# Kernel optimization log

Hardware: AMD Instinct MI355X
Metric: run time of the kernel (lower is better)

Reference implementation:

```python
import jax, jax.numpy as jnp
import numpy as np

B, L, D, H = 4, 2048, 256, 8
FF = 128  # ff_intermediary_depth hard-coded in module
EPS = 1e-5


def layer_norm(x, g, b):
    mu = jnp.mean(x, axis=-1, keepdims=True)
    var = jnp.mean(jnp.square(x - mu), axis=-1, keepdims=True)
    return (x - mu) * jax.lax.rsqrt(var + EPS) * g + b


def setup_inputs() -> dict:
    key = jax.random.key(0)
    ks = jax.random.split(key, 8)
    s = 1.0 / np.sqrt(D)
    return {
        "seq": jax.random.normal(ks[0], (B, L, D), dtype=jnp.float32),
        "Wq": jax.random.normal(ks[1], (D, D * H), dtype=jnp.float32) * s,
        "Wk": jax.random.normal(ks[2], (D, D * H), dtype=jnp.float32) * s,
        "Wv": jax.random.normal(ks[3], (D, D * H), dtype=jnp.float32) * s,
        "Wo": jax.random.normal(ks[4], (D * H, D), dtype=jnp.float32) * (1.0 / np.sqrt(D * H)),
        "ln1_g": jnp.ones((D,), jnp.float32),
        "ln1_b": jnp.zeros((D,), jnp.float32),
        "W1": jax.random.normal(ks[5], (D, FF), dtype=jnp.float32) * s,
        "b1": jnp.zeros((FF,), jnp.float32),
        "W2": jax.random.normal(ks[6], (FF, D), dtype=jnp.float32) * (1.0 / np.sqrt(FF)),
        "b2": jnp.zeros((D,), jnp.float32),
        "ln2_g": jnp.ones((D,), jnp.float32),
        "ln2_b": jnp.zeros((D,), jnp.float32),
    }


def reference(seq, Wq, Wk, Wv, Wo, ln1_g, ln1_b, W1, b1, W2, b2, ln2_g, ln2_b):
    b, l, d = seq.shape
    # per-head dim equals full depth d (module quirk)
    q = (seq @ Wq).reshape(b, l, H, d)
    k = (seq @ Wk).reshape(b, l, H, d)
    v = (seq @ Wv).reshape(b, l, H, d)
    scores = jnp.einsum('bqhd,bkhd->bhqk', q, k) / jnp.sqrt(jnp.float32(d))
    a = jax.nn.softmax(scores, axis=-1)
    heads = jnp.einsum('bhqk,bkhd->bqhd', a, v).reshape(b, l, H * d)
    att_out = heads @ Wo
    x = layer_norm(seq + att_out, ln1_g, ln1_b)
    ff = jax.nn.relu(x @ W1 + b1) @ W2 + b2
    return layer_norm(x + ff, ln2_g, ln2_b)
```

## Files before the change

kernel.cpp:

```cpp
#include <hip/hip_runtime.h>


typedef unsigned short u16;
typedef unsigned int   u32;
typedef __bf16 bf16x8 __attribute__((ext_vector_type(8)));
typedef float  f32x4  __attribute__((ext_vector_type(4)));

#define MFMA(a, b, c) __builtin_amdgcn_mfma_f32_16x16x32_bf16(a, b, c, 0, 0, 0)

__device__ __forceinline__ float b2f(u16 h) {
  return __uint_as_float(((u32)h) << 16);
}
__device__ __forceinline__ u16 f2b(float f) {
  u32 u = __float_as_uint(f);
  u += 0x7FFFu + ((u >> 16) & 1u);
  return (u16)(u >> 16);
}
__device__ __forceinline__ bf16x8 ldb8(const u16* p) { return *(const bf16x8*)p; }

typedef const __attribute__((address_space(1))) u32* gas1_t;
typedef __attribute__((address_space(3))) u32* las3_t;
__device__ __forceinline__ void gload_lds16(const u16* g, u16* lds_base) {
  __builtin_amdgcn_global_load_lds((gas1_t)(const void*)g,
                                   (las3_t)(void*)lds_base, 16, 0, 0);
}

__device__ __forceinline__ int detect_f32(const void* seq) {
  const u32* s = (const u32*)seq;
  int cnt = 0;
  #pragma unroll
  for (int i = 0; i < 64; i++) {
    u32 e = (s[i] >> 7) & 0xFFu;
    cnt += (e >= 100u && e <= 140u) ? 1 : 0;
  }
  return cnt < 48;
}

__device__ __forceinline__ u16 ldw(const void* W, size_t idx, int isf32) {
  return isf32 ? f2b(((const float*)W)[idx]) : ((const u16*)W)[idx];
}

__global__ __launch_bounds__(256) void ingest_kernel(
    const void* __restrict__ seq, const void* __restrict__ g1,
    const void* __restrict__ be1, const void* __restrict__ b1,
    const void* __restrict__ b2v, const void* __restrict__ g2,
    const void* __restrict__ be2, u16* __restrict__ sbuf,
    u16* __restrict__ vecs) {
  int isf32 = detect_f32(seq);
  int bx = blockIdx.x, tid = threadIdx.x;
  if (bx < 2048) {
    size_t i = (size_t)bx * 1024 + tid * 4;
    if (isf32) {
      const float* sp = (const float*)seq;
      u16 o0 = f2b(sp[i]), o1 = f2b(sp[i + 1]), o2 = f2b(sp[i + 2]), o3 = f2b(sp[i + 3]);
      uint2 ov; ov.x = (u32)o0 | ((u32)o1 << 16); ov.y = (u32)o2 | ((u32)o3 << 16);
      *(uint2*)(sbuf + i) = ov;
    } else {
      *(uint2*)(sbuf + i) = ((const uint2*)seq)[i >> 2];
    }
  } else {
    int t = bx - 2048;
    const void* src; int n;
    switch (t) {
      case 0: src = g1;  n = 256; break;
      case 1: src = be1; n = 256; break;
      case 2: src = b1;  n = 128; break;
      case 3: src = b2v; n = 256; break;
      case 4: src = g2;  n = 256; break;
      default: src = be2; n = 256; break;
    }
    if (tid < n) vecs[t * 256 + tid] = ldw(src, tid, isf32);
  }
}

__global__ __launch_bounds__(256) void pack_kernel(
    const void* __restrict__ Wq, const void* __restrict__ Wk,
    const void* __restrict__ Wv, const void* __restrict__ Wo,
    const void* __restrict__ W1, const void* __restrict__ W2,
    const void* __restrict__ seq,
    u16* __restrict__ pWq, u16* __restrict__ pWk, u16* __restrict__ pWv,
    u16* __restrict__ pWo, u16* __restrict__ pW1, u16* __restrict__ pW2) {
  int isf32 = detect_f32(seq);
  const void* W; u16* P; int K, N;
  switch (blockIdx.y) {
    case 0: W = Wq; P = pWq; K = 256;  N = 2048; break;
    case 1: W = Wk; P = pWk; K = 256;  N = 2048; break;
    case 2: W = Wv; P = pWv; K = 256;  N = 2048; break;
    case 3: W = Wo; P = pWo; K = 2048; N = 256;  break;
    case 4: W = W1; P = pW1; K = 256;  N = 128;  break;
    default: W = W2; P = pW2; K = 128; N = 256;  break;
  }
  int t = blockIdx.x * 256 + threadIdx.x;
  int total = (K >> 5) * (N >> 4) * 64;
  if (t >= total) return;
  int lane = t & 63, f = t >> 6;
  int NT = N >> 4;
  int kt = f / NT, nt = f - kt * NT;
  int row0 = kt * 32 + ((lane >> 4) << 3);
  int col = nt * 16 + (lane & 15);
  u16 e[8];
  #pragma unroll
  for (int j = 0; j < 8; j++) e[j] = ldw(W, (size_t)(row0 + j) * N + col, isf32);
  uint4 u;
  u.x = (u32)e[0] | ((u32)e[1] << 16);
  u.y = (u32)e[2] | ((u32)e[3] << 16);
  u.z = (u32)e[4] | ((u32)e[5] << 16);
  u.w = (u32)e[6] | ((u32)e[7] << 16);
  *(uint4*)(P + ((size_t)f * 64 + lane) * 8) = u;
}

__global__ __launch_bounds__(256) void qkv_kernel(
    const u16* __restrict__ X,
    const u16* __restrict__ pWq, const u16* __restrict__ pWk,
    const u16* __restrict__ pWv,
    u16* __restrict__ Qo, u16* __restrict__ Ko, u16* __restrict__ Vo,
    int ntbase, int hc) {
  __shared__ u16 blds[64 * 512];
  const u16* Pw = (blockIdx.z == 0) ? pWq : ((blockIdx.z == 1) ? pWk : pWv);
  u16* Out = (blockIdx.z == 0) ? Qo : ((blockIdx.z == 1) ? Ko : Vo);
  int tid = threadIdx.x, lane = tid & 63, w = tid >> 6;
  int nt0 = ntbase + blockIdx.x * 8;
  #pragma unroll
  for (int i = 0; i < 16; i++) {
    int u = tid + i * 256;
    int fl = u >> 6, q = u & 63;
    int kt = fl >> 3, nt = fl & 7;
    ((uint4*)blds)[u] = ((const uint4*)Pw)[(size_t)(kt * 128 + nt0 + nt) * 64 + q];
  }
  __syncthreads();
  int m0 = blockIdx.y * 128 + w * 32;
  f32x4 acc[2][8] = {};
  #pragma unroll
  for (int kt = 0; kt < 8; kt++) {
    bf16x8 a0 = ldb8(X + (size_t)(m0 + (lane & 15)) * 256 + kt * 32 + (lane >> 4) * 8);
    bf16x8 a1 = ldb8(X + (size_t)(m0 + 16 + (lane & 15)) * 256 + kt * 32 + (lane >> 4) * 8);
    const u16* bp = blds + (size_t)kt * 8 * 512 + (size_t)lane * 8;
    #pragma unroll
    for (int nt = 0; nt < 8; nt++) {
      bf16x8 b = ldb8(bp + nt * 512);
      acc[0][nt] = MFMA(a0, b, acc[0][nt]);
      acc[1][nt] = MFMA(a1, b, acc[1][nt]);
    }
  }
  int isv = (blockIdx.z == 2);
  int hl = blockIdx.x >> 1;
  int dd0 = (blockIdx.x & 1) * 128;
  int m0b = blockIdx.y * 128;
  int bi = m0b >> 11, l0 = m0b & 2047;
  __syncthreads();
  if (!isv) {
    #pragma unroll
    for (int mt = 0; mt < 2; mt++)
      #pragma unroll
      for (int nt = 0; nt < 8; nt++)
        #pragma unroll
        for (int r = 0; r < 4; r++)
          blds[(w * 32 + mt * 16 + (lane >> 4) * 4 + r) * 136 + nt * 16 + (lane & 15)] =
              f2b(acc[mt][nt][r]);
    __syncthreads();
    #pragma unroll
    for (int i = 0; i < 8; i++) {
      int c = tid + i * 256;
      int mloc = c >> 4, q = c & 15;
      uint4 v = *(uint4*)(blds + mloc * 136 + q * 8);
      *(uint4*)(Out + ((size_t)(bi * hc + hl) * 2048 + l0 + mloc) * 256 + dd0 + q * 8) = v;
    }
  } else {
    #pragma unroll
    for (int mt = 0; mt < 2; mt++)
      #pragma unroll
      for (int nt = 0; nt < 8; nt++)
        #pragma unroll
        for (int r = 0; r < 4; r++)
          blds[(nt * 16 + (lane & 15)) * 136 + w * 32 + mt * 16 + (lane >> 4) * 4 + r] =
              f2b(acc[mt][nt][r]);
    __syncthreads();
    #pragma unroll
    for (int i = 0; i < 8; i++) {
      int c = tid + i * 256;
      int nloc = c >> 4, q = c & 15;
      uint4 v = *(uint4*)(blds + nloc * 136 + q * 8);
      *(uint4*)(Out + ((size_t)(bi * hc + hl) * 256 + dd0 + nloc) * 2048 + l0 + q * 8) = v;
    }
  }
}

__global__ __launch_bounds__(512, 4) void attn_kernel(
    const u16* __restrict__ Q, const u16* __restrict__ K,
    const u16* __restrict__ Vt, u16* __restrict__ O, int nbh) {
  __shared__ u16 kbuf[2 * 8192];
  __shared__ u16 vbuf[2 * 8192];
  __shared__ u16 plds[8 * 640];
  int tid = threadIdx.x, lane = tid & 63, w = tid >> 6;
  int bi2 = blockIdx.x;
  int bh, qt;
  if (nbh >= 8) {
    int G = nbh >> 3;
    bh = (bi2 & 7) * G + (bi2 >> 3) % G;
    qt = bi2 / (8 * G);
  } else {
    bh = bi2 % nbh; qt = bi2 / nbh;
  }
  const u16* Qb  = Q  + (size_t)bh * 2048 * 256;
  const u16* Kb  = K  + (size_t)bh * 2048 * 256;
  const u16* Vtb = Vt + (size_t)bh * 256 * 2048;
  u16* Ob = O + (size_t)bh * 2048 * 256;
  int q0 = qt * 128 + w * 16;
  bf16x8 qf[8];
  #pragma unroll
  for (int kt = 0; kt < 8; kt++)
    qf[kt] = ldb8(Qb + (size_t)(q0 + (lane & 15)) * 256 + kt * 32 + (lane >> 4) * 8);
  f32x4 o[16] = {};
  float lsum = 0.f;
  const float cexp = 0.0625f * 1.44269504088896f;
  u16* pl = plds + (size_t)w * 640;

  #pragma unroll
  for (int j = 0; j < 2; j++) {
    int f = w * 2 + j;
    gload_lds16(Kb + (size_t)((f >> 3) * 16 + (lane & 15)) * 256 +
                    (f & 7) * 32 + (lane >> 4) * 8,
                kbuf + f * 512);
    gload_lds16(Vtb + (size_t)(f * 16 + (lane & 15)) * 2048 + (lane >> 4) * 8,
                vbuf + f * 512);
  }

  for (int t = 0; t < 64; t++) {
    int s0 = t * 32;
    asm volatile("s_waitcnt vmcnt(0)\ns_barrier" ::: "memory");
    if (t < 63) {
      int nb = (t + 1) & 1;
      #pragma unroll
      for (int j = 0; j < 2; j++) {
        int f = w * 2 + j;
        gload_lds16(Kb + (size_t)(s0 + 32 + (f >> 3) * 16 + (lane & 15)) * 256 +
                        (f & 7) * 32 + (lane >> 4) * 8,
                    kbuf + nb * 8192 + f * 512);
        gload_lds16(Vtb + (size_t)(f * 16 + (lane & 15)) * 2048 + s0 + 32 +
                        (lane >> 4) * 8,
                    vbuf + nb * 8192 + f * 512);
      }
    }
    const u16* kb = kbuf + (t & 1) * 8192;
    f32x4 s[2] = {};
    #pragma unroll
    for (int ntk = 0; ntk < 2; ntk++)
      #pragma unroll
      for (int kt = 0; kt < 8; kt++) {
        bf16x8 a = ldb8(kb + (size_t)(ntk * 8 + kt) * 512 + lane * 8);
        s[ntk] = MFMA(a, qf[kt], s[ntk]);
      }
    #pragma unroll
    for (int ntk = 0; ntk < 2; ntk++) {
      float p0 = exp2f(s[ntk][0] * cexp);
      float p1 = exp2f(s[ntk][1] * cexp);
      float p2 = exp2f(s[ntk][2] * cexp);
      float p3 = exp2f(s[ntk][3] * cexp);
      lsum += (p0 + p1) + (p2 + p3);
      uint2 pk;
      pk.x = (u32)f2b(p0) | ((u32)f2b(p1) << 16);
      pk.y = (u32)f2b(p2) | ((u32)f2b(p3) << 16);
      *(uint2*)(pl + (lane & 15) * 40 + 16 * ntk + 4 * (lane >> 4)) = pk;
    }
    asm volatile("s_waitcnt lgkmcnt(0)" ::: "memory");
    bf16x8 pa = ldb8(pl + (lane & 15) * 40 + (lane >> 4) * 8);
    const u16* vb0 = vbuf + (t & 1) * 8192;
    #pragma unroll
    for (int nt = 0; nt < 16; nt++) {
      bf16x8 vb = ldb8(vb0 + (size_t)nt * 512 + lane * 8);
      o[nt] = MFMA(vb, pa, o[nt]);
    }
  }
  float l = lsum;
  l += __shfl_xor(l, 16);
  l += __shfl_xor(l, 32);
  float linv = 1.0f / l;
  u16* el = kbuf + w * 1152;
  __syncthreads();
  #pragma unroll
  for (int g = 0; g < 4; g++) {
    if (g) asm volatile("s_waitcnt lgkmcnt(0)" ::: "memory");
    #pragma unroll
    for (int t = 0; t < 4; t++) {
      int nt = g * 4 + t;
      uint2 pk;
      pk.x = (u32)f2b(o[nt][0] * linv) | ((u32)f2b(o[nt][1] * linv) << 16);
      pk.y = (u32)f2b(o[nt][2] * linv) | ((u32)f2b(o[nt][3] * linv) << 16);
      *(uint2*)(el + (lane & 15) * 72 + t * 16 + 4 * (lane >> 4)) = pk;
    }
    asm volatile("s_waitcnt lgkmcnt(0)" ::: "memory");
    #pragma unroll
    for (int rep = 0; rep < 2; rep++) {
      int ch = lane + rep * 64;
      int row = ch >> 3, c8 = ch & 7;
      uint4 v = *(uint4*)(el + row * 72 + c8 * 8);
      *(uint4*)(Ob + (size_t)(q0 + row) * 256 + g * 64 + c8 * 8) = v;
    }
  }
}

__global__ __launch_bounds__(256) void accum_ln1_kernel(
    const u16* __restrict__ Oc, const u16* __restrict__ pWo,
    const u16* __restrict__ sbuf, const u16* __restrict__ vecs,
    u16* __restrict__ xout) {
  __shared__ u16 blds[64 * 512];
  int tid = threadIdx.x, lane = tid & 63, w = tid >> 6;
  int m0 = blockIdx.x * 64 + w * 16;
  int arow = m0 + (lane & 15);
  int bq = arow >> 11, lrow = arow & 2047;
  f32x4 acc[16] = {};
  for (int k0 = 0; k0 < 64; k0 += 4) {
    __syncthreads();
    #pragma unroll
    for (int i = 0; i < 16; i++) {
      int u = tid + i * 256;
      int fl = u >> 6, q = u & 63;
      int ktg = k0 + (fl >> 4), nt = fl & 15;
      ((uint4*)blds)[u] = ((const uint4*)pWo)[(size_t)(ktg * 16 + nt) * 64 + q];
    }
    __syncthreads();
    #pragma unroll
    for (int kl = 0; kl < 4; kl++) {
      int ktl = k0 + kl;
      int hl = ktl >> 3;
      int d0 = (ktl & 7) * 32 + (lane >> 4) * 8;
      bf16x8 a = ldb8(Oc + ((size_t)(bq * 8 + hl) * 2048 + lrow) * 256 + d0);
      const u16* bp = blds + (size_t)kl * 16 * 512 + (size_t)lane * 8;
      #pragma unroll
      for (int nt = 0; nt < 16; nt++) {
        bf16x8 b = ldb8(bp + nt * 512);
        acc[nt] = MFMA(a, b, acc[nt]);
      }
    }
  }
  int rbase = m0 + (lane >> 4) * 4;
  #pragma unroll
  for (int nt = 0; nt < 16; nt++) {
    int d = nt * 16 + (lane & 15);
    #pragma unroll
    for (int r = 0; r < 4; r++)
      acc[nt][r] += b2f(sbuf[(size_t)(rbase + r) * 256 + d]);
  }
  float mu[4], rs[4];
  #pragma unroll
  for (int r = 0; r < 4; r++) {
    float sm = 0.f;
    #pragma unroll
    for (int nt = 0; nt < 16; nt++) sm += acc[nt][r];
    sm += __shfl_xor(sm, 1); sm += __shfl_xor(sm, 2);
    sm += __shfl_xor(sm, 4); sm += __shfl_xor(sm, 8);
    mu[r] = sm * (1.0f / 256.0f);
    float v = 0.f;
    #pragma unroll
    for (int nt = 0; nt < 16; nt++) { float dd = acc[nt][r] - mu[r]; v += dd * dd; }
    v += __shfl_xor(v, 1); v += __shfl_xor(v, 2);
    v += __shfl_xor(v, 4); v += __shfl_xor(v, 8);
    rs[r] = rsqrtf(v * (1.0f / 256.0f) + 1e-5f);
  }
  #pragma unroll
  for (int nt = 0; nt < 16; nt++) {
    int d = nt * 16 + (lane & 15);
    float gg = b2f(vecs[d]), bb = b2f(vecs[256 + d]);
    #pragma unroll
    for (int r = 0; r < 4; r++)
      xout[(size_t)(rbase + r) * 256 + d] = f2b((acc[nt][r] - mu[r]) * rs[r] * gg + bb);
  }
}

__global__ __launch_bounds__(256) void accum_kernel(
    const u16* __restrict__ Oc, const u16* __restrict__ pWo,
    float* __restrict__ att_out, int kt0, int hc) {
  __shared__ u16 blds[64 * 512];
  int tid = threadIdx.x, lane = tid & 63, w = tid >> 6;
  int m0 = blockIdx.x * 64 + w * 16;
  int arow = m0 + (lane & 15);
  int bq = arow >> 11, lrow = arow & 2047;
  int ktn = hc * 8;
  f32x4 acc[16] = {};
  for (int k0 = 0; k0 < ktn; k0 += 4) {
    __syncthreads();
    #pragma unroll
    for (int i = 0; i < 16; i++) {
      int u = tid + i * 256;
      int fl = u >> 6, q = u & 63;
      int ktg = kt0 + k0 + (fl >> 4), nt = fl & 15;
      ((uint4*)blds)[u] = ((const uint4*)pWo)[(size_t)(ktg * 16 + nt) * 64 + q];
    }
    __syncthreads();
    #pragma unroll
    for (int kl = 0; kl < 4; kl++) {
      int ktl = k0 + kl;
      int hl = ktl >> 3;
      int d0 = (ktl & 7) * 32 + (lane >> 4) * 8;
      bf16x8 a = ldb8(Oc + ((size_t)(bq * hc + hl) * 2048 + lrow) * 256 + d0);
      const u16* bp = blds + (size_t)kl * 16 * 512 + (size_t)lane * 8;
      #pragma unroll
      for (int nt = 0; nt < 16; nt++) {
        bf16x8 b = ldb8(bp + nt * 512);
        acc[nt] = MFMA(a, b, acc[nt]);
      }
    }
  }
  int rbase = m0 + (lane >> 4) * 4;
  #pragma unroll
  for (int nt = 0; nt < 16; nt++) {
    int d = nt * 16 + (lane & 15);
    #pragma unroll
    for (int r = 0; r < 4; r++)
      att_out[(size_t)(rbase + r) * 256 + d] += acc[nt][r];
  }
}

__global__ __launch_bounds__(256) void ln1_kernel(
    const float* __restrict__ att_out, const u16* __restrict__ sbuf,
    const u16* __restrict__ vecs, u16* __restrict__ xout) {
  int tid = threadIdx.x, lane = tid & 63, w = tid >> 6;
  int row = blockIdx.x * 4 + w;
  const float* ar = att_out + (size_t)row * 256;
  f32x4 a = *(const f32x4*)(ar + lane * 4);
  uint2 sv = *(const uint2*)(sbuf + (size_t)row * 256 + lane * 4);
  float y[4];
  y[0] = a[0] + b2f((u16)(sv.x & 0xFFFF));
  y[1] = a[1] + b2f((u16)(sv.x >> 16));
  y[2] = a[2] + b2f((u16)(sv.y & 0xFFFF));
  y[3] = a[3] + b2f((u16)(sv.y >> 16));
  float sm = y[0] + y[1] + y[2] + y[3];
  sm += __shfl_xor(sm, 1);  sm += __shfl_xor(sm, 2);  sm += __shfl_xor(sm, 4);
  sm += __shfl_xor(sm, 8);  sm += __shfl_xor(sm, 16); sm += __shfl_xor(sm, 32);
  float mu = sm * (1.0f / 256.0f);
  float v = 0.f;
  #pragma unroll
  for (int j = 0; j < 4; j++) { float d = y[j] - mu; v += d * d; }
  v += __shfl_xor(v, 1);  v += __shfl_xor(v, 2);  v += __shfl_xor(v, 4);
  v += __shfl_xor(v, 8);  v += __shfl_xor(v, 16); v += __shfl_xor(v, 32);
  float rs = rsqrtf(v * (1.0f / 256.0f) + 1e-5f);
  u16 o[4];
  #pragma unroll
  for (int j = 0; j < 4; j++) {
    int d = lane * 4 + j;
    o[j] = f2b((y[j] - mu) * rs * b2f(vecs[d]) + b2f(vecs[256 + d]));
  }
  uint2 ov; ov.x = (u32)o[0] | ((u32)o[1] << 16); ov.y = (u32)o[2] | ((u32)o[3] << 16);
  *(uint2*)(xout + (size_t)row * 256 + lane * 4) = ov;
}

__global__ __launch_bounds__(256) void ffn_ln2_kernel(
    const u16* __restrict__ x, const u16* __restrict__ pW1,
    const u16* __restrict__ pW2, const u16* __restrict__ vecs,
    const void* __restrict__ seq, void* __restrict__ out) {
  __shared__ u16 hbuf[4 * 16 * 136];
  int isf32 = detect_f32(seq);
  int tid = threadIdx.x, lane = tid & 63, w = tid >> 6;
  int m0 = blockIdx.x * 64 + w * 16;
  int arow = m0 + (lane & 15);
  u16* hb = hbuf + w * 16 * 136;
  f32x4 acc1[8] = {};
  #pragma unroll
  for (int kt = 0; kt < 8; kt++) {
    bf16x8 a = ldb8(x + (size_t)arow * 256 + kt * 32 + (lane >> 4) * 8);
    const u16* bp = pW1 + ((size_t)kt * 8 * 64 + lane) * 8;
    #pragma unroll
    for (int nt = 0; nt < 8; nt++) {
      bf16x8 b = ldb8(bp + nt * 512);
      acc1[nt] = MFMA(a, b, acc1[nt]);
    }
  }
  #pragma unroll
  for (int nt = 0; nt < 8; nt++) {
    int col = nt * 16 + (lane & 15);
    float bb = b2f(vecs[512 + col]);
    #pragma unroll
    for (int r = 0; r < 4; r++) {
      float h = fmaxf(acc1[nt][r] + bb, 0.f);
      hb[((lane >> 4) * 4 + r) * 136 + col] = f2b(h);
    }
  }
  __syncthreads();
  f32x4 acc2[16] = {};
  #pragma unroll
  for (int ks = 0; ks < 4; ks++) {
    bf16x8 a = ldb8(hb + (lane & 15) * 136 + ks * 32 + (lane >> 4) * 8);
    const u16* bp = pW2 + ((size_t)ks * 16 * 64 + lane) * 8;
    #pragma unroll
    for (int nt = 0; nt < 16; nt++) {
      bf16x8 b = ldb8(bp + nt * 512);
      acc2[nt] = MFMA(a, b, acc2[nt]);
    }
  }
  int rbase = m0 + (lane >> 4) * 4;
  #pragma unroll
  for (int nt = 0; nt < 16; nt++) {
    int d = nt * 16 + (lane & 15);
    float bb = b2f(vecs[768 + d]);
    #pragma unroll
    for (int r = 0; r < 4; r++)
      acc2[nt][r] += bb + b2f(x[(size_t)(rbase + r) * 256 + d]);
  }
  float mu[4], rs[4];
  #pragma unroll
  for (int r = 0; r < 4; r++) {
    float sm = 0.f;
    #pragma unroll
    for (int nt = 0; nt < 16; nt++) sm += acc2[nt][r];
    sm += __shfl_xor(sm, 1); sm += __shfl_xor(sm, 2);
    sm += __shfl_xor(sm, 4); sm += __shfl_xor(sm, 8);
    mu[r] = sm * (1.0f / 256.0f);
    float v = 0.f;
    #pragma unroll
    for (int nt = 0; nt < 16; nt++) { float dd = acc2[nt][r] - mu[r]; v += dd * dd; }
    v += __shfl_xor(v, 1); v += __shfl_xor(v, 2);
    v += __shfl_xor(v, 4); v += __shfl_xor(v, 8);
    rs[r] = rsqrtf(v * (1.0f / 256.0f) + 1e-5f);
  }
  #pragma unroll
  for (int nt = 0; nt < 16; nt++) {
    int d = nt * 16 + (lane & 15);
    float gg = b2f(vecs[1024 + d]), bb = b2f(vecs[1280 + d]);
    #pragma unroll
    for (int r = 0; r < 4; r++) {
      float val = (acc2[nt][r] - mu[r]) * rs[r] * gg + bb;
      size_t idx = (size_t)(rbase + r) * 256 + d;
      if (isf32) ((float*)out)[idx] = val;
      else       ((u16*)out)[idx]   = f2b(val);
    }
  }
}

__global__ __launch_bounds__(256) void sentinel_kernel(void* out, int n,
                                                       const void* seq) {
  int isf32 = detect_f32(seq);
  int i = blockIdx.x * 256 + threadIdx.x;
  if (i < n) {
    if (isf32) ((float*)out)[i] = 777.0f;
    else       ((u16*)out)[i]   = 0x4442;
  }
}

extern "C" void kernel_launch(void* const* d_in, const int* in_sizes, int n_in,
                              void* d_out, int out_size, void* d_ws, size_t ws_size,
                              hipStream_t stream) {
  (void)in_sizes; (void)n_in;
  const void* seq  = d_in[0];
  const void* Wq   = d_in[1];
  const void* Wk   = d_in[2];
  const void* Wv   = d_in[3];
  const void* Wo   = d_in[4];
  const void* g1   = d_in[5];
  const void* be1  = d_in[6];
  const void* W1   = d_in[7];
  const void* b1   = d_in[8];
  const void* W2   = d_in[9];
  const void* b2   = d_in[10];
  const void* g2   = d_in[11];
  const void* be2  = d_in[12];

  size_t o = 0;
  u16* ws = (u16*)d_ws;
  u16* pWq = ws + o; o += 524288;
  u16* pWk = ws + o; o += 524288;
  u16* pWv = ws + o; o += 524288;
  u16* pWo = ws + o; o += 524288;
  u16* pW1 = ws + o; o += 32768;
  u16* pW2 = ws + o; o += 32768;
  float* att = (float*)(ws + o); o += 4194304;
  u16* xb   = ws + o; o += 2097152;
  u16* sbuf = ws + o; o += 2097152;
  u16* vecs = ws + o; o += 2048;
  size_t fixed_elems = o;

  int hc = 0;
  for (int c = 8; c >= 1; c >>= 1) {
    size_t need = (fixed_elems + (size_t)4 * c * 2097152) * 2;
    if (need <= ws_size) { hc = c; break; }
  }
  if (hc == 0) {
    sentinel_kernel<<<dim3((out_size + 255) / 256), 256, 0, stream>>>(
        d_out, out_size, seq);
    return;
  }
  u16* Qc = ws + o; o += (size_t)hc * 2097152;
  u16* Kc = ws + o; o += (size_t)hc * 2097152;
  u16* Vc = ws + o; o += (size_t)hc * 2097152;
  u16* Oc = ws + o;

  ingest_kernel<<<dim3(2054), 256, 0, stream>>>(seq, g1, be1, b1, b2, g2, be2,
                                                sbuf, vecs);
  pack_kernel<<<dim3(256, 6), 256, 0, stream>>>(Wq, Wk, Wv, Wo, W1, W2, seq,
                                                pWq, pWk, pWv, pWo, pW1, pW2);
  if (hc == 8) {
    qkv_kernel<<<dim3(16, 64, 3), 256, 0, stream>>>(
        sbuf, pWq, pWk, pWv, Qc, Kc, Vc, 0, 8);
    attn_kernel<<<dim3(32 * 16), 512, 0, stream>>>(Qc, Kc, Vc, Oc, 32);
    accum_ln1_kernel<<<dim3(128), 256, 0, stream>>>(Oc, pWo, sbuf, vecs, xb);
  } else {
    hipMemsetAsync(att, 0, 2097152 * sizeof(float), stream);
    int nchunks = 8 / hc;
    for (int c = 0; c < nchunks; c++) {
      int nbh = 4 * hc;
      qkv_kernel<<<dim3(2 * hc, 64, 3), 256, 0, stream>>>(
          sbuf, pWq, pWk, pWv, Qc, Kc, Vc, c * hc * 16, hc);
      attn_kernel<<<dim3(nbh * 16), 512, 0, stream>>>(Qc, Kc, Vc, Oc, nbh);
      accum_kernel<<<dim3(128), 256, 0, stream>>>(Oc, pWo, att, c * hc * 8, hc);
    }
    ln1_kernel<<<dim3(2048), 256, 0, stream>>>(att, sbuf, vecs, xb);
  }
  ffn_ln2_kernel<<<dim3(128), 256, 0, stream>>>(xb, pW1, pW2, vecs, seq,
                                                (void*)d_out);
}
```

Baseline: 370.8 us.

## Have each attention wave process two query tiles to reuse K/V fragments

The attention kernel now runs 4 waves per block instead of 8. Each wave owns 32 query rows (two 16-row MFMA tiles), so every K and V fragment read from LDS feeds two MFMAs. Each wave issues twice as many async global-to-LDS loads, and s_setprio hints are placed around the MFMA phases. In exchange, each wave holds twice the accumulator and Q registers, and there are fewer waves per block to hide latency.

Result: no change. 372.7 us (+0.5%).

```diff
diff --git a/kernel.cpp b/kernel.cpp
--- a/kernel.cpp
+++ b/kernel.cpp
@@ -185,12 +185,12 @@
   }
 }
 
-__global__ __launch_bounds__(512, 4) void attn_kernel(
+__global__ __launch_bounds__(256, 2) void attn_kernel(
     const u16* __restrict__ Q, const u16* __restrict__ K,
     const u16* __restrict__ Vt, u16* __restrict__ O, int nbh) {
   __shared__ u16 kbuf[2 * 8192];
   __shared__ u16 vbuf[2 * 8192];
-  __shared__ u16 plds[8 * 640];
+  __shared__ u16 plds[4 * 1280];
   int tid = threadIdx.x, lane = tid & 63, w = tid >> 6;
   int bi2 = blockIdx.x;
   int bh, qt;
@@ -205,19 +205,22 @@
   const u16* Kb  = K  + (size_t)bh * 2048 * 256;
   const u16* Vtb = Vt + (size_t)bh * 256 * 2048;
   u16* Ob = O + (size_t)bh * 2048 * 256;
-  int q0 = qt * 128 + w * 16;
-  bf16x8 qf[8];
-  #pragma unroll
-  for (int kt = 0; kt < 8; kt++)
-    qf[kt] = ldb8(Qb + (size_t)(q0 + (lane & 15)) * 256 + kt * 32 + (lane >> 4) * 8);
-  f32x4 o[16] = {};
-  float lsum = 0.f;
+  int q0 = qt * 128 + w * 32;
+  bf16x8 qf[2][8];
+  #pragma unroll
+  for (int qq = 0; qq < 2; qq++)
+    #pragma unroll
+    for (int kt = 0; kt < 8; kt++)
+      qf[qq][kt] = ldb8(Qb + (size_t)(q0 + qq * 16 + (lane & 15)) * 256 +
+                        kt * 32 + (lane >> 4) * 8);
+  f32x4 o[2][16] = {};
+  float lsum[2] = {0.f, 0.f};
   const float cexp = 0.0625f * 1.44269504088896f;
-  u16* pl = plds + (size_t)w * 640;
-
-  #pragma unroll
-  for (int j = 0; j < 2; j++) {
-    int f = w * 2 + j;
+  u16* pl = plds + (size_t)w * 1280;
+
+  #pragma unroll
+  for (int j = 0; j < 4; j++) {
+    int f = w * 4 + j;
     gload_lds16(Kb + (size_t)((f >> 3) * 16 + (lane & 15)) * 256 +
                     (f & 7) * 32 + (lane >> 4) * 8,
                 kbuf + f * 512);
@@ -231,8 +234,8 @@
     if (t < 63) {
       int nb = (t + 1) & 1;
       #pragma unroll
-      for (int j = 0; j < 2; j++) {
-        int f = w * 2 + j;
+      for (int j = 0; j < 4; j++) {
+        int f = w * 4 + j;
         gload_lds16(Kb + (size_t)(s0 + 32 + (f >> 3) * 16 + (lane & 15)) * 256 +
                         (f & 7) * 32 + (lane >> 4) * 8,
                     kbuf + nb * 8192 + f * 512);
@@ -242,59 +245,71 @@
       }
     }
     const u16* kb = kbuf + (t & 1) * 8192;
-    f32x4 s[2] = {};
+    f32x4 s[2][2] = {};
+    __builtin_amdgcn_s_setprio(1);
     #pragma unroll
     for (int ntk = 0; ntk < 2; ntk++)
       #pragma unroll
       for (int kt = 0; kt < 8; kt++) {
         bf16x8 a = ldb8(kb + (size_t)(ntk * 8 + kt) * 512 + lane * 8);
-        s[ntk] = MFMA(a, qf[kt], s[ntk]);
+        s[0][ntk] = MFMA(a, qf[0][kt], s[0][ntk]);
+        s[1][ntk] = MFMA(a, qf[1][kt], s[1][ntk]);
       }
-    #pragma unroll
-    for (int ntk = 0; ntk < 2; ntk++) {
-      float p0 = exp2f(s[ntk][0] * cexp);
-      float p1 = exp2f(s[ntk][1] * cexp);
-      float p2 = exp2f(s[ntk][2] * cexp);
-      float p3 = exp2f(s[ntk][3] * cexp);
-      lsum += (p0 + p1) + (p2 + p3);
-      uint2 pk;
-      pk.x = (u32)f2b(p0) | ((u32)f2b(p1) << 16);
-      pk.y = (u32)f2b(p2) | ((u32)f2b(p3) << 16);
-      *(uint2*)(pl + (lane & 15) * 40 + 16 * ntk + 4 * (lane >> 4)) = pk;
-    }
+    __builtin_amdgcn_s_setprio(0);
+    #pragma unroll
+    for (int qq = 0; qq < 2; qq++)
+      #pragma unroll
+      for (int ntk = 0; ntk < 2; ntk++) {
+        float p0 = exp2f(s[qq][ntk][0] * cexp);
+        float p1 = exp2f(s[qq][ntk][1] * cexp);
+        float p2 = exp2f(s[qq][ntk][2] * cexp);
+        float p3 = exp2f(s[qq][ntk][3] * cexp);
+        lsum[qq] += (p0 + p1) + (p2 + p3);
+        uint2 pk;
+        pk.x = (u32)f2b(p0) | ((u32)f2b(p1) << 16);
+        pk.y = (u32)f2b(p2) | ((u32)f2b(p3) << 16);
+        *(uint2*)(pl + (qq * 16 + (lane & 15)) * 40 + 16 * ntk + 4 * (lane >> 4)) = pk;
+      }
     asm volatile("s_waitcnt lgkmcnt(0)" ::: "memory");
-    bf16x8 pa = ldb8(pl + (lane & 15) * 40 + (lane >> 4) * 8);
+    bf16x8 pa0 = ldb8(pl + (lane & 15) * 40 + (lane >> 4) * 8);
+    bf16x8 pa1 = ldb8(pl + (16 + (lane & 15)) * 40 + (lane >> 4) * 8);
     const u16* vb0 = vbuf + (t & 1) * 8192;
+    __builtin_amdgcn_s_setprio(1);
     #pragma unroll
     for (int nt = 0; nt < 16; nt++) {
       bf16x8 vb = ldb8(vb0 + (size_t)nt * 512 + lane * 8);
-      o[nt] = MFMA(vb, pa, o[nt]);
-    }
-  }
-  float l = lsum;
-  l += __shfl_xor(l, 16);
-  l += __shfl_xor(l, 32);
-  float linv = 1.0f / l;
+      o[0][nt] = MFMA(vb, pa0, o[0][nt]);
+      o[1][nt] = MFMA(vb, pa1, o[1][nt]);
+    }
+    __builtin_amdgcn_s_setprio(0);
+  }
   u16* el = kbuf + w * 1152;
   __syncthreads();
   #pragma unroll
-  for (int g = 0; g < 4; g++) {
-    if (g) asm volatile("s_waitcnt lgkmcnt(0)" ::: "memory");
-    #pragma unroll
-    for (int t = 0; t < 4; t++) {
-      int nt = g * 4 + t;
-      uint2 pk;
-      pk.x = (u32)f2b(o[nt][0] * linv) | ((u32)f2b(o[nt][1] * linv) << 16);
-      pk.y = (u32)f2b(o[nt][2] * linv) | ((u32)f2b(o[nt][3] * linv) << 16);
-      *(uint2*)(el + (lane & 15) * 72 + t * 16 + 4 * (lane >> 4)) = pk;
-    }
-    asm volatile("s_waitcnt lgkmcnt(0)" ::: "memory");
-    #pragma unroll
-    for (int rep = 0; rep < 2; rep++) {
-      int ch = lane + rep * 64;
-      int row = ch >> 3, c8 = ch & 7;
-      uint4 v = *(uint4*)(el + row * 72 + c8 * 8);
-      *(uint4*)(Ob + (size_t)(q0 + row) * 256 + g * 64 + c8 * 8) = v;
+  for (int qq = 0; qq < 2; qq++) {
+    float l = lsum[qq];
+    l += __shfl_xor(l, 16);
+    l += __shfl_xor(l, 32);
+    float linv = 1.0f / l;
+    #pragma unroll
+    for (int g = 0; g < 4; g++) {
+      if (qq || g) asm volatile("s_waitcnt lgkmcnt(0)" ::: "memory");
+      #pragma unroll
+      for (int t2 = 0; t2 < 4; t2++) {
+        int nt = g * 4 + t2;
+        uint2 pk;
+        pk.x = (u32)f2b(o[qq][nt][0] * linv) | ((u32)f2b(o[qq][nt][1] * linv) << 16);
+        pk.y = (u32)f2b(o[qq][nt][2] * linv) | ((u32)f2b(o[qq][nt][3] * linv) << 16);
+        *(uint2*)(el + (lane & 15) * 72 + t2 * 16 + 4 * (lane >> 4)) = pk;
+      }
+      asm volatile("s_waitcnt lgkmcnt(0)" ::: "memory");
+      #pragma unroll
+      for (int rep = 0; rep < 2; rep++) {
+        int ch = lane + rep * 64;
+        int row = ch >> 3, c8 = ch & 7;
+        uint4 v = *(uint4*)(el + row * 72 + c8 * 8);
+        *(uint4*)(Ob + (size_t)(q0 + qq * 16 + row) * 256 + g * 64 + c8 * 8) = v;
+      }
     }
   }
 }
@@ -590,7 +605,7 @@
   if (hc == 8) {
     qkv_kernel<<<dim3(16, 64, 3), 256, 0, stream>>>(
         sbuf, pWq, pWk, pWv, Qc, Kc, Vc, 0, 8);
-    attn_kernel<<<dim3(32 * 16), 512, 0, stream>>>(Qc, Kc, Vc, Oc, 32);
+    attn_kernel<<<dim3(32 * 16), 256, 0, stream>>>(Qc, Kc, Vc, Oc, 32);
     accum_ln1_kernel<<<dim3(128), 256, 0, stream>>>(Oc, pWo, sbuf, vecs, xb);
   } else {
     hipMemsetAsync(att, 0, 2097152 * sizeof(float), stream);
@@ -599,7 +614,7 @@
       int nbh = 4 * hc;
       qkv_kernel<<<dim3(2 * hc, 64, 3), 256, 0, stream>>>(
           sbuf, pWq, pWk, pWv, Qc, Kc, Vc, c * hc * 16, hc);
-      attn_kernel<<<dim3(nbh * 16), 512, 0, stream>>>(Qc, Kc, Vc, Oc, nbh);
+      attn_kernel<<<dim3(nbh * 16), 256, 0, stream>>>(Qc, Kc, Vc, Oc, nbh);
       accum_kernel<<<dim3(128), 256, 0, stream>>>(Oc, pWo, att, c * hc * 8, hc);
     }
     ln1_kernel<<<dim3(2048), 256, 0, stream>>>(att, sbuf, vecs, xb);
```
